# Kernel tuning notes

Measured on AMD Instinct MI355X. Metric: run time of the kernel, lower is better.

The kernel has to match this reference:

```python
import jax, jax.numpy as jnp
import numpy as np

N = 8192          # batch_size == number of graph nodes
F1 = 64
F2 = 64
D_IN = F1 * F2    # 4096, = int(sqrt(in_feats))**2
D_OUT = 4096      # out_feats, must equal F1*F2 for the final reshape
ALPHA = 0.2       # LeakyReLU negative slope


def setup_inputs() -> dict:
    key = jax.random.key(0)
    k_x, k_w, k_a = jax.random.split(key, 3)
    x = jax.random.normal(k_x, (N, F1, F2), dtype=jnp.float32)
    # torch Linear weight layout: [out_feats, in_feats]; xavier-uniform-ish scale
    lim_w = float(np.sqrt(6.0 / (D_IN + D_OUT)) * np.sqrt(2.0))
    W = jax.random.uniform(k_w, (D_OUT, D_IN), dtype=jnp.float32, minval=-lim_w, maxval=lim_w)
    lim_a = float(np.sqrt(6.0 / (1 + 2 * D_OUT)))
    a = jax.random.uniform(k_a, (1, 2 * D_OUT), dtype=jnp.float32, minval=-lim_a, maxval=lim_a)
    return {"x": x, "W": W, "a": a}


def reference(x, W, a):
    b, f1, f2 = x.shape
    x_flat = x.reshape(b, f1 * f2)                 # [N, D_in]
    h = x_flat @ W.T                               # [N, D_out]
    # scores[i,j] = leakyrelu(cat(h_i, h_j) @ a.T) = leakyrelu(h_i.a1 + h_j.a2)
    a1 = a[0, :D_OUT]                              # [D_out]
    a2 = a[0, D_OUT:]                              # [D_out]
    s1 = h @ a1                                    # [N]
    s2 = h @ a2                                    # [N]
    e = s1[:, None] + s2[None, :]                  # [N, N]
    e = jnp.where(e > 0, e, ALPHA * e)             # LeakyReLU
    attention = jax.nn.softmax(e, axis=-1)         # [N, N]
    # dropout=0.0 (eval-mode / deterministic reference)
    out = attention @ h                            # [N, D_out]
    return out.reshape(b, f1, f2)
```

## Files before the change

### kernel.cpp

```cpp
#include <hip/hip_runtime.h>
#include <hip/hip_bf16.h>
#include <stdint.h>


typedef float  f32x4  __attribute__((ext_vector_type(4)));
typedef __bf16 bf16x8 __attribute__((ext_vector_type(8)));

#define AS1 __attribute__((address_space(1)))
#define AS3 __attribute__((address_space(3)))

constexpr int NB  = 8192;
constexpr int DF  = 4096;
constexpr int CH  = 64;
constexpr int NCH = NB / CH;

constexpr int GK  = DF;
constexpr int BKK = 64;
constexpr int NT2 = GK / BKK;

__device__ __forceinline__ uint16_t f2bf_u(float f) {
  union { float f; uint32_t u; } x; x.f = f;
  return (uint16_t)((x.u + 0x7FFFu + ((x.u >> 16) & 1u)) >> 16);
}
__device__ __forceinline__ float bfu2f(uint16_t v) {
  union { uint32_t u; float f; } x; x.u = ((uint32_t)v) << 16;
  return x.f;
}

__global__ __launch_bounds__(256) void cvt_f32_to_bf16(
    const float* __restrict__ in, uint16_t* __restrict__ out, int n4,
    float* __restrict__ z1, float* __restrict__ z2, int zn) {
  int idx = blockIdx.x * 256 + threadIdx.x;
  int stride = gridDim.x * 256;
  if (z1) {
    for (int g = idx; g < zn; g += stride) { z1[g] = 0.f; z2[g] = 0.f; }
  }
  for (int i = idx; i < n4; i += stride) {
    float4 v = ((const float4*)in)[i];
    ushort4 o;
    o.x = f2bf_u(v.x); o.y = f2bf_u(v.y); o.z = f2bf_u(v.z); o.w = f2bf_u(v.w);
    ((ushort4*)out)[i] = o;
  }
}


#define STAGE_A(tt, half) do {                                                 \
  const uint16_t* g0_ = Ag + (size_t)((half) * 128) * GK + (size_t)(tt) * BKK; \
  uint32_t d_ = ((uint32_t)((tt) & 1)) * 32768u + (uint32_t)(half) * 8192u +   \
                (uint32_t)wave * 512u;                                         \
  __builtin_amdgcn_global_load_lds((const AS1 void*)g0_,                       \
      (AS3 void*)(lds + d_), 16, 0, 0);                                        \
  __builtin_amdgcn_global_load_lds((const AS1 void*)(g0_ + (size_t)64 * GK),   \
      (AS3 void*)(lds + d_ + 4096u), 16, 0, 0);                                \
} while (0)

#define STAGE_B(tt, half) do {                                                 \
  const uint16_t* g0_ = Bg + (size_t)((half) * 128) * GK + (size_t)(tt) * BKK; \
  uint32_t d_ = ((uint32_t)((tt) & 1)) * 32768u + 16384u +                     \
                (uint32_t)(half) * 8192u + (uint32_t)wave * 512u;              \
  __builtin_amdgcn_global_load_lds((const AS1 void*)g0_,                       \
      (AS3 void*)(lds + d_), 16, 0, 0);                                        \
  __builtin_amdgcn_global_load_lds((const AS1 void*)(g0_ + (size_t)64 * GK),   \
      (AS3 void*)(lds + d_ + 4096u), 16, 0, 0);                                \
} while (0)

#define LDA(mh) do {                                                           \
  _Pragma("unroll") for (int mf = 0; mf < 4; ++mf)                             \
    _Pragma("unroll") for (int ks = 0; ks < 2; ++ks)                           \
      aF[mf][ks] = *(const bf16x8*)(lds + bufo +                               \
          (uint32_t)(wm * 128 + (mh) * 64 + mf * 16 + lr) * 64u +              \
          (uint32_t)((ks * 32 + lg * 8) ^ swl));                               \
} while (0)

#define LDB(nh) do {                                                           \
  _Pragma("unroll") for (int nf = 0; nf < 2; ++nf)                             \
    _Pragma("unroll") for (int ks = 0; ks < 2; ++ks)                           \
      bF[nf][ks] = *(const bf16x8*)(lds + bufo + 16384u +                      \
          (uint32_t)(wn * 64 + (nh) * 32 + nf * 16 + lr) * 64u +               \
          (uint32_t)((ks * 32 + lg * 8) ^ swl));                               \
} while (0)

#define MMA(mh, nh) do {                                                       \
  _Pragma("unroll") for (int ks = 0; ks < 2; ++ks)                             \
    _Pragma("unroll") for (int mf = 0; mf < 4; ++mf)                           \
      _Pragma("unroll") for (int nf = 0; nf < 2; ++nf)                         \
        acc[(mh) * 4 + mf][(nh) * 2 + nf] =                                    \
            __builtin_amdgcn_mfma_f32_16x16x32_bf16(aF[mf][ks], bF[nf][ks],    \
                acc[(mh) * 4 + mf][(nh) * 2 + nf], 0, 0, 0);                   \
} while (0)

__global__ __launch_bounds__(512, 2) void gemm_nt_async(
    const uint16_t* __restrict__ A, const uint16_t* __restrict__ B,
    uint16_t* __restrict__ C, const float* __restrict__ a,
    float* __restrict__ s1g, float* __restrict__ s2g) {
  __shared__ uint16_t lds[65536];

  const int tid  = threadIdx.x;
  const int wave = tid >> 6;
  const int lane = tid & 63;
  const int lr   = lane & 15;
  const int lg   = lane >> 4;
  const int wm   = wave >> 2;
  const int wn   = wave & 3;
  const int swl  = (lr & 7) << 3;

  const int bid = blockIdx.x;
  const int swz = (bid & 7) * 64 + (bid >> 3);
  const int bx  = swz & 15;
  const int by  = swz >> 4;
  const int rowBase = by * 256;
  const int colBase = bx * 256;

  const int sr  = tid >> 3;
  const int sch = (tid & 7) ^ (sr & 7);
  const uint16_t* Ag = A + (size_t)(rowBase + sr) * GK + sch * 8;
  const uint16_t* Bg = B + (size_t)(colBase + sr) * GK + sch * 8;

  f32x4 acc[8][4];
#pragma unroll
  for (int mf = 0; mf < 8; ++mf)
#pragma unroll
    for (int nf = 0; nf < 4; ++nf) acc[mf][nf] = (f32x4){0.f, 0.f, 0.f, 0.f};

  STAGE_A(0, 0);
  STAGE_A(0, 1);
  STAGE_B(0, 0);
  STAGE_B(0, 1);
  asm volatile("s_waitcnt vmcnt(0)" ::: "memory");
  __builtin_amdgcn_s_barrier();

  bf16x8 aF[4][2], bF[2][2];

  for (int t = 0; t < NT2; ++t) {
    const uint32_t bufo = ((uint32_t)(t & 1)) * 32768u;

    if (t + 1 < NT2) {
      STAGE_A(t + 1, 0);
      STAGE_A(t + 1, 1);
      STAGE_B(t + 1, 0);
      STAGE_B(t + 1, 1);
    }

    LDA(0); LDB(0);
    MMA(0, 0);
    LDB(1);
    MMA(0, 1);
    LDA(1);
    MMA(1, 1);
    LDB(0);
    MMA(1, 0);

    if (t + 1 < NT2) {
      asm volatile("s_waitcnt vmcnt(0)" ::: "memory");
      __builtin_amdgcn_s_barrier();
    }
  }

  const int r0 = rowBase + wm * 128 + lg * 4;
  const int c0 = colBase + wn * 64 + lr;
#pragma unroll
  for (int mf = 0; mf < 8; ++mf)
#pragma unroll
    for (int nf = 0; nf < 4; ++nf)
#pragma unroll
      for (int e = 0; e < 4; ++e)
        C[(size_t)(r0 + mf * 16 + e) * (size_t)DF + (c0 + nf * 16)] =
            f2bf_u(acc[mf][nf][e]);

  float a1v[4], a2v[4];
#pragma unroll
  for (int nf = 0; nf < 4; ++nf) {
    int col = c0 + nf * 16;
    a1v[nf] = a[col];
    a2v[nf] = a[DF + col];
  }
#pragma unroll
  for (int mf = 0; mf < 8; ++mf) {
#pragma unroll
    for (int e = 0; e < 4; ++e) {
      float p1 = 0.f, p2 = 0.f;
#pragma unroll
      for (int nf = 0; nf < 4; ++nf) {
        float hv = acc[mf][nf][e];
        p1 += hv * a1v[nf];
        p2 += hv * a2v[nf];
      }
      p1 += __shfl_xor(p1, 1, 64); p1 += __shfl_xor(p1, 2, 64);
      p1 += __shfl_xor(p1, 4, 64); p1 += __shfl_xor(p1, 8, 64);
      p2 += __shfl_xor(p2, 1, 64); p2 += __shfl_xor(p2, 2, 64);
      p2 += __shfl_xor(p2, 4, 64); p2 += __shfl_xor(p2, 8, 64);
      if (lr == 0) {
        int row = r0 + mf * 16 + e;
        atomicAdd(&s1g[row], p1);
        atomicAdd(&s2g[row], p2);
      }
    }
  }
}

__global__ __launch_bounds__(256) void rankcount_kernel(
    const float* __restrict__ s1, const float* __restrict__ s2,
    int* __restrict__ pi, float* __restrict__ s2sorted, int* __restrict__ ci) {
  __shared__ float ld[NB];
  const int t = threadIdx.x;
  for (int idx = t; idx < NB; idx += 256) ld[idx] = s2[idx];
  __syncthreads();
  const int i    = blockIdx.x * 64 + (t >> 2);
  const int part = t & 3;
  const float v   = ld[i];
  const float thr = -s1[i];
  int cr = 0, cc = 0;
  const int q0 = part * (NB / 16);
  for (int q = q0; q < q0 + NB / 16; q++) {
    float4 u = ((const float4*)ld)[q];
    int jj = q * 4;
    cr += (u.x > v) || (u.x == v && (jj + 0) < i);
    cr += (u.y > v) || (u.y == v && (jj + 1) < i);
    cr += (u.z > v) || (u.z == v && (jj + 2) < i);
    cr += (u.w > v) || (u.w == v && (jj + 3) < i);
    cc += (u.x > thr) + (u.y > thr) + (u.z > thr) + (u.w > thr);
  }
  cr += __shfl_xor(cr, 1, 64); cr += __shfl_xor(cr, 2, 64);
  cc += __shfl_xor(cc, 1, 64); cc += __shfl_xor(cc, 2, 64);
  if (part == 0) {
    pi[cr] = i;
    s2sorted[cr] = v;
    ci[i] = cc;
  }
}

__global__ __launch_bounds__(256) void mega_kernel(
    const float* __restrict__ s2sorted, float* __restrict__ Sb,
    float* __restrict__ Sc, float* __restrict__ wbg, float* __restrict__ wcg,
    const float* __restrict__ s1, const int* __restrict__ ci,
    float* __restrict__ f1, float* __restrict__ f2,
    int* __restrict__ istart, int* __restrict__ cursor) {
  __shared__ float pb[256], pc[256];
  __shared__ int   histL[NB + 1];
  __shared__ int   ps[256];
  const int t = threadIdx.x;
  for (int g = t; g <= NB; g += 256) histL[g] = 0;

  float sb = 0.f, sc = 0.f;
  for (int c = t * 32; c < t * 32 + 32; c++) {
    float s = s2sorted[c];
    float wb = __expf(0.2f * s), wc = __expf(s);
    wbg[c] = wb; wcg[c] = wc;
    sb += wb; sc += wc;
  }
  pb[t] = sb; pc[t] = sc;
  __syncthreads();
  if (t == 0) {
    float rb = 0.f, rc = 0.f;
    for (int q = 0; q < 256; q++) {
      float tb = pb[q], tc = pc[q];
      pb[q] = rb; pc[q] = rc;
      rb += tb; rc += tc;
    }
    Sb[0] = 0.f; Sc[0] = 0.f;
    Sb[NB] = rb; Sc[NB] = rc;
  }
  __syncthreads();
  {
    float rb = pb[t], rc = pc[t];
    for (int c = t * 32; c < t * 32 + 32; c++) {
      rb += wbg[c]; rc += wcg[c];
      if (c + 1 < NB) { Sb[c + 1] = rb; Sc[c + 1] = rc; }
    }
  }
  __syncthreads();

  const float SbT = Sb[NB];
  for (int q = 0; q < NB / 256; q++) {
    int i = q * 256 + t;
    float s1i = s1[i];
    int c = ci[i];
    float q1 = __expf(0.2f * s1i), q2 = __expf(s1i);
    float l = q1 * (SbT - Sb[c]) + q2 * Sc[c];
    f1[i] = q1 / l;
    f2[i] = q2 / l;
    atomicAdd(&histL[c], 1);
  }
  __syncthreads();

  {
    const int lo = t * 33;
    const int hi = min(lo + 33, NB + 1);
    int s = 0;
    for (int b = lo; b < hi; b++) s += histL[b];
    ps[t] = s;
    __syncthreads();
    if (t == 0) {
      int r = 0;
      for (int q = 0; q < 256; q++) { int v = ps[q]; ps[q] = r; r += v; }
    }
    __syncthreads();
    int r = ps[t];
    for (int b = lo; b < hi; b++) { istart[b] = r; cursor[b] = r; r += histL[b]; }
    if (t == 255) istart[NB + 1] = r;
  }
}

__global__ __launch_bounds__(256) void pass1_kernel(
    const uint16_t* __restrict__ h, const int* __restrict__ pi,
    const float* __restrict__ wbg, const float* __restrict__ wcg,
    float* __restrict__ Bct, float* __restrict__ Cct,
    const int* __restrict__ ci, int* __restrict__ cursor,
    int* __restrict__ ilist) {
  __shared__ int   pj[CH];
  __shared__ float wb[CH], wc[CH];
  const int t  = threadIdx.x;
  const int cb = blockIdx.x;
  const int k  = blockIdx.y;
  const int flat = k * 4 + cb;
  if (flat < 32) {
    const int i = flat * 256 + t;
    const int b = ci[i];
    const int pos = atomicAdd(&cursor[b], 1);
    ilist[pos] = i;
  }
  if (t < CH) {
    int g = k * CH + t;
    pj[t] = pi[g]; wb[t] = wbg[g]; wc[t] = wcg[g];
  }
  __syncthreads();
  const int n0 = cb * 1024 + t * 4;
  float b0 = 0.f, b1 = 0.f, b2 = 0.f, b3 = 0.f;
  float c0 = 0.f, c1 = 0.f, c2 = 0.f, c3 = 0.f;
#pragma unroll 8
  for (int c = 0; c < CH; c++) {
    uint2 hv = *(const uint2*)(h + (size_t)pj[c] * DF + n0);
    float h0 = bfu2f((uint16_t)hv.x), h1 = bfu2f((uint16_t)(hv.x >> 16));
    float h2 = bfu2f((uint16_t)hv.y), h3 = bfu2f((uint16_t)(hv.y >> 16));
    float vb = wb[c], vc = wc[c];
    b0 += vb * h0; b1 += vb * h1; b2 += vb * h2; b3 += vb * h3;
    c0 += vc * h0; c1 += vc * h1; c2 += vc * h2; c3 += vc * h3;
  }
  *(float4*)(Bct + (size_t)k * DF + n0) = make_float4(b0, b1, b2, b3);
  *(float4*)(Cct + (size_t)k * DF + n0) = make_float4(c0, c1, c2, c3);
}

__global__ __launch_bounds__(256) void boff_kernel(
    const float* __restrict__ Bct, const float* __restrict__ Cct,
    float* __restrict__ Boff, float* __restrict__ Coff) {
  __shared__ float sB[4][64], sC[4][64];
  const int t   = threadIdx.x;
  const int cl  = t & 63;
  const int seg = t >> 6;
  const int col = blockIdx.x * 64 + cl;
  float sb = 0.f, sc = 0.f;
#pragma unroll 8
  for (int u = 0; u < NCH / 4; u++) {
    int kk = seg * (NCH / 4) + u;
    sb += Bct[(size_t)kk * DF + col];
    sc += Cct[(size_t)kk * DF + col];
  }
  sB[seg][cl] = sb; sC[seg][cl] = sc;
  __syncthreads();
  float rb = 0.f, rc = 0.f;
#pragma unroll
  for (int s = 0; s < 3; s++)
    if (s < seg) { rb += sB[s][cl]; rc += sC[s][cl]; }
#pragma unroll 4
  for (int u = 0; u < NCH / 4; u++) {
    int kk = seg * (NCH / 4) + u;
    Boff[(size_t)kk * DF + col] = rb;
    Coff[(size_t)kk * DF + col] = rc;
    rb += Bct[(size_t)kk * DF + col];
    rc += Cct[(size_t)kk * DF + col];
  }
  if (seg == 3) {
    Boff[(size_t)NCH * DF + col] = rb;
    Coff[(size_t)NCH * DF + col] = rc;
  }
}

__global__ __launch_bounds__(256) void pass2_kernel(
    const uint16_t* __restrict__ h, const int* __restrict__ pi,
    const float* __restrict__ wbg, const float* __restrict__ wcg,
    const float* __restrict__ Boff, const float* __restrict__ Coff,
    const int* __restrict__ istart, const int* __restrict__ ilist,
    const float* __restrict__ f1, const float* __restrict__ f2,
    float* __restrict__ out) {
  __shared__ int   pj[CH];
  __shared__ float wb[CH], wc[CH];
  __shared__ int   se[CH + 2];
  const int t  = threadIdx.x;
  const int cb = blockIdx.x;
  const int k  = blockIdx.y;
  if (t < CH) {
    int g = k * CH + t;
    pj[t] = pi[g]; wb[t] = wbg[g]; wc[t] = wcg[g];
  }
  if (t < CH + 2) se[t] = istart[k * CH + t];
  __syncthreads();
  const int n0 = cb * 1024 + t * 4;
  const float4 An = *(const float4*)(Boff + (size_t)NCH * DF + n0);
  const float4 Bo = *(const float4*)(Boff + (size_t)k * DF + n0);
  const float4 Co = *(const float4*)(Coff + (size_t)k * DF + n0);
  float b0 = Bo.x, b1 = Bo.y, b2 = Bo.z, b3 = Bo.w;
  float c0 = Co.x, c1 = Co.y, c2 = Co.z, c3 = Co.w;

  if (k == 0) {
    for (int idx = se[0]; idx < se[1]; idx++) {
      const int i = ilist[idx];
      const float fa = f1[i];
      *(float4*)(out + (size_t)i * DF + n0) =
          make_float4(fa * An.x, fa * An.y, fa * An.z, fa * An.w);
    }
  }
  for (int c = 0; c < CH; c++) {
    uint2 hv = *(const uint2*)(h + (size_t)pj[c] * DF + n0);
    float h0 = bfu2f((uint16_t)hv.x), h1 = bfu2f((uint16_t)(hv.x >> 16));
    float h2 = bfu2f((uint16_t)hv.y), h3 = bfu2f((uint16_t)(hv.y >> 16));
    float vb = wb[c], vc = wc[c];
    b0 += vb * h0; b1 += vb * h1; b2 += vb * h2; b3 += vb * h3;
    c0 += vc * h0; c1 += vc * h1; c2 += vc * h2; c3 += vc * h3;
    const int e0 = se[c + 1], e1 = se[c + 2];
    for (int idx = e0; idx < e1; idx++) {
      const int i = ilist[idx];
      const float fa = f1[i], fb = f2[i];
      *(float4*)(out + (size_t)i * DF + n0) = make_float4(
          fa * (An.x - b0) + fb * c0, fa * (An.y - b1) + fb * c1,
          fa * (An.z - b2) + fb * c2, fa * (An.w - b3) + fb * c3);
    }
  }
}

extern "C" void kernel_launch(void* const* d_in, const int* in_sizes, int n_in,
                              void* d_out, int out_size, void* d_ws, size_t ws_size,
                              hipStream_t stream) {
  const float* x = (const float*)d_in[0];
  const float* W = (const float*)d_in[1];
  const float* a = (const float*)d_in[2];
  float* out = (float*)d_out;

  char* ws = (char*)d_ws;
  uint16_t* h = (uint16_t*)ws;
  char* sm = ws + 67108864;
  float* s1       = (float*)(sm);
  float* s2       = (float*)(sm + 65536);
  float* s2sorted = (float*)(sm + 131072);
  int*   pi       = (int*)  (sm + 196608);
  int*   ci       = (int*)  (sm + 262144);
  float* Sb       = (float*)(sm + 327680);
  float* Sc       = (float*)(sm + 393216);
  float* wbg      = (float*)(sm + 458752);
  float* wcg      = (float*)(sm + 524288);
  float* f1       = (float*)(sm + 589824);
  float* f2       = (float*)(sm + 655360);
  int*   istart   = (int*)  (sm + 786432);
  int*   cursor   = (int*)  (sm + 851968);
  int*   ilist    = (int*)  (sm + 917504);
  float* Bct      = (float*)(sm + 1048576);
  float* Cct      = (float*)(sm + 3145728);
  float* Boff     = (float*)(sm + 5242880);
  float* Coff     = (float*)(sm + 7602176);
  char* base2 = ws + 67108864 + 10485760;
  uint16_t* xb = (uint16_t*)base2;
  uint16_t* Wb = (uint16_t*)(base2 + 67108864);

  cvt_f32_to_bf16<<<1024, 256, 0, stream>>>(x, xb, (NB * DF) / 4, s1, s2, NB);
  cvt_f32_to_bf16<<<1024, 256, 0, stream>>>(W, Wb, (DF * DF) / 4,
                                            nullptr, nullptr, 0);

  gemm_nt_async<<<(NB / 256) * (DF / 256), 512, 0, stream>>>(
      xb, Wb, h, a, s1, s2);

  rankcount_kernel<<<NB / 64, 256, 0, stream>>>(s1, s2, pi, s2sorted, ci);

  mega_kernel<<<1, 256, 0, stream>>>(s2sorted, Sb, Sc, wbg, wcg,
                                     s1, ci, f1, f2, istart, cursor);

  pass1_kernel<<<dim3(DF / 1024, NCH), 256, 0, stream>>>(
      h, pi, wbg, wcg, Bct, Cct, ci, cursor, ilist);

  boff_kernel<<<DF / 64, 256, 0, stream>>>(Bct, Cct, Boff, Coff);

  pass2_kernel<<<dim3(DF / 1024, NCH), 256, 0, stream>>>(
      h, pi, wbg, wcg, Boff, Coff, istart, ilist, f1, f2, out);
}
```

Measured before the change: 723.8 us.

## Fuse post-GEMM stages into one cooperative kernel with grid syncs

```diff
diff --git a/kernel.cpp b/kernel.cpp
--- a/kernel.cpp
+++ b/kernel.cpp
@@ -1,6 +1,9 @@
 #include <hip/hip_runtime.h>
 #include <hip/hip_bf16.h>
+#include <hip/hip_cooperative_groups.h>
 #include <stdint.h>
+
+namespace cg = cooperative_groups;
 
 
 typedef float  f32x4  __attribute__((ext_vector_type(4)));
@@ -27,19 +30,23 @@
   return x.f;
 }
 
-__global__ __launch_bounds__(256) void cvt_f32_to_bf16(
-    const float* __restrict__ in, uint16_t* __restrict__ out, int n4,
-    float* __restrict__ z1, float* __restrict__ z2, int zn) {
-  int idx = blockIdx.x * 256 + threadIdx.x;
-  int stride = gridDim.x * 256;
-  if (z1) {
-    for (int g = idx; g < zn; g += stride) { z1[g] = 0.f; z2[g] = 0.f; }
-  }
-  for (int i = idx; i < n4; i += stride) {
-    float4 v = ((const float4*)in)[i];
+__global__ __launch_bounds__(256) void cvt_all(
+    const float* __restrict__ x, uint16_t* __restrict__ xb,
+    const float* __restrict__ W, uint16_t* __restrict__ Wb) {
+  const int idx = blockIdx.x * 256 + threadIdx.x;
+  const int stride = gridDim.x * 256;
+  const int n4x = (NB * DF) / 4, n4w = (DF * DF) / 4;
+  for (int i = idx; i < n4x; i += stride) {
+    float4 v = ((const float4*)x)[i];
     ushort4 o;
     o.x = f2bf_u(v.x); o.y = f2bf_u(v.y); o.z = f2bf_u(v.z); o.w = f2bf_u(v.w);
-    ((ushort4*)out)[i] = o;
+    ((ushort4*)xb)[i] = o;
+  }
+  for (int i = idx; i < n4w; i += stride) {
+    float4 v = ((const float4*)W)[i];
+    ushort4 o;
+    o.x = f2bf_u(v.x); o.y = f2bf_u(v.y); o.z = f2bf_u(v.z); o.w = f2bf_u(v.w);
+    ((ushort4*)Wb)[i] = o;
   }
 }
 
@@ -92,7 +99,7 @@
 __global__ __launch_bounds__(512, 2) void gemm_nt_async(
     const uint16_t* __restrict__ A, const uint16_t* __restrict__ B,
     uint16_t* __restrict__ C, const float* __restrict__ a,
-    float* __restrict__ s1g, float* __restrict__ s2g) {
+    float* __restrict__ s1p, float* __restrict__ s2p) {
   __shared__ uint16_t lds[65536];
 
   const int tid  = threadIdx.x;
@@ -174,6 +181,7 @@
     a1v[nf] = a[col];
     a2v[nf] = a[DF + col];
   }
+  const int q = bx * 4 + wn;
 #pragma unroll
   for (int mf = 0; mf < 8; ++mf) {
 #pragma unroll
@@ -191,238 +199,247 @@
       p2 += __shfl_xor(p2, 4, 64); p2 += __shfl_xor(p2, 8, 64);
       if (lr == 0) {
         int row = r0 + mf * 16 + e;
-        atomicAdd(&s1g[row], p1);
-        atomicAdd(&s2g[row], p2);
-      }
-    }
-  }
-}
-
-__global__ __launch_bounds__(256) void rankcount_kernel(
-    const float* __restrict__ s1, const float* __restrict__ s2,
-    int* __restrict__ pi, float* __restrict__ s2sorted, int* __restrict__ ci) {
-  __shared__ float ld[NB];
-  const int t = threadIdx.x;
-  for (int idx = t; idx < NB; idx += 256) ld[idx] = s2[idx];
-  __syncthreads();
-  const int i    = blockIdx.x * 64 + (t >> 2);
-  const int part = t & 3;
-  const float v   = ld[i];
-  const float thr = -s1[i];
-  int cr = 0, cc = 0;
-  const int q0 = part * (NB / 16);
-  for (int q = q0; q < q0 + NB / 16; q++) {
-    float4 u = ((const float4*)ld)[q];
-    int jj = q * 4;
-    cr += (u.x > v) || (u.x == v && (jj + 0) < i);
-    cr += (u.y > v) || (u.y == v && (jj + 1) < i);
-    cr += (u.z > v) || (u.z == v && (jj + 2) < i);
-    cr += (u.w > v) || (u.w == v && (jj + 3) < i);
-    cc += (u.x > thr) + (u.y > thr) + (u.z > thr) + (u.w > thr);
-  }
-  cr += __shfl_xor(cr, 1, 64); cr += __shfl_xor(cr, 2, 64);
-  cc += __shfl_xor(cc, 1, 64); cc += __shfl_xor(cc, 2, 64);
-  if (part == 0) {
-    pi[cr] = i;
-    s2sorted[cr] = v;
-    ci[i] = cc;
-  }
-}
-
-__global__ __launch_bounds__(256) void mega_kernel(
-    const float* __restrict__ s2sorted, float* __restrict__ Sb,
-    float* __restrict__ Sc, float* __restrict__ wbg, float* __restrict__ wcg,
-    const float* __restrict__ s1, const int* __restrict__ ci,
-    float* __restrict__ f1, float* __restrict__ f2,
-    int* __restrict__ istart, int* __restrict__ cursor) {
-  __shared__ float pb[256], pc[256];
-  __shared__ int   histL[NB + 1];
-  __shared__ int   ps[256];
-  const int t = threadIdx.x;
-  for (int g = t; g <= NB; g += 256) histL[g] = 0;
-
-  float sb = 0.f, sc = 0.f;
-  for (int c = t * 32; c < t * 32 + 32; c++) {
-    float s = s2sorted[c];
-    float wb = __expf(0.2f * s), wc = __expf(s);
-    wbg[c] = wb; wcg[c] = wc;
-    sb += wb; sc += wc;
-  }
-  pb[t] = sb; pc[t] = sc;
-  __syncthreads();
-  if (t == 0) {
+        s1p[(size_t)q * NB + row] = p1;
+        s2p[(size_t)q * NB + row] = p2;
+      }
+    }
+  }
+}
+
+
+struct PostArgs {
+  const uint16_t* h;
+  const float* s1p; const float* s2p;
+  float* s1; float* s2;
+  int* pi; float* s2sorted; int* ci;
+  float* Sb; float* Sc; float* wbg; float* wcg;
+  float* f1; float* f2;
+  int* istart; int* cursor; int* ilist;
+  float* Bct; float* Cct; float* Boff; float* Coff;
+  float* out;
+};
+
+union PostSmem {
+  float ld[NB];
+  struct { float pb[256]; float pc[256]; int histL[NB + 1]; int ps[256]; } mg;
+  struct { int pj[CH]; float wb[CH]; float wc[CH]; int se[CH + 2]; } pp;
+  struct { float sB[4][64]; float sC[4][64]; } bo;
+};
+
+__global__ __launch_bounds__(256, 2) void gat_post(PostArgs P) {
+  __shared__ PostSmem smu;
+  cg::grid_group grid = cg::this_grid();
+  const int bid = blockIdx.x;
+  const int t   = threadIdx.x;
+
+  if (bid < 32) {
+    const int i = bid * 256 + t;
+    float v1 = 0.f, v2 = 0.f;
+#pragma unroll 16
+    for (int q = 0; q < 64; q++) {
+      v1 += P.s1p[(size_t)q * NB + i];
+      v2 += P.s2p[(size_t)q * NB + i];
+    }
+    P.s1[i] = v1;
+    P.s2[i] = v2;
+  }
+  grid.sync();
+
+  {
+    for (int idx = t; idx < NB; idx += 256) smu.ld[idx] = P.s2[idx];
+    __syncthreads();
+    const int i    = bid * 16 + (t >> 4);
+    const int part = t & 15;
+    const float v   = smu.ld[i];
+    const float thr = -P.s1[i];
+    int cr = 0, cc = 0;
+    const int q0 = part * (NB / 64);
+    for (int q = q0; q < q0 + NB / 64; q++) {
+      float4 u = ((const float4*)smu.ld)[q];
+      int jj = q * 4;
+      cr += (u.x > v) || (u.x == v && (jj + 0) < i);
+      cr += (u.y > v) || (u.y == v && (jj + 1) < i);
+      cr += (u.z > v) || (u.z == v && (jj + 2) < i);
+      cr += (u.w > v) || (u.w == v && (jj + 3) < i);
+      cc += (u.x > thr) + (u.y > thr) + (u.z > thr) + (u.w > thr);
+    }
+    cr += __shfl_xor(cr, 1, 64); cr += __shfl_xor(cr, 2, 64);
+    cr += __shfl_xor(cr, 4, 64); cr += __shfl_xor(cr, 8, 64);
+    cc += __shfl_xor(cc, 1, 64); cc += __shfl_xor(cc, 2, 64);
+    cc += __shfl_xor(cc, 4, 64); cc += __shfl_xor(cc, 8, 64);
+    if (part == 0) {
+      P.pi[cr] = i;
+      P.s2sorted[cr] = v;
+      P.ci[i] = cc;
+    }
+  }
+  grid.sync();
+
+  if (bid == 0) {
+    for (int g = t; g <= NB; g += 256) smu.mg.histL[g] = 0;
+    float sb = 0.f, sc = 0.f;
+    for (int c = t * 32; c < t * 32 + 32; c++) {
+      float s = P.s2sorted[c];
+      float wb = __expf(0.2f * s), wc = __expf(s);
+      P.wbg[c] = wb; P.wcg[c] = wc;
+      sb += wb; sc += wc;
+    }
+    smu.mg.pb[t] = sb; smu.mg.pc[t] = sc;
+    __syncthreads();
+    if (t == 0) {
+      float rb = 0.f, rc = 0.f;
+      for (int q = 0; q < 256; q++) {
+        float tb = smu.mg.pb[q], tc = smu.mg.pc[q];
+        smu.mg.pb[q] = rb; smu.mg.pc[q] = rc;
+        rb += tb; rc += tc;
+      }
+      P.Sb[0] = 0.f; P.Sc[0] = 0.f;
+      P.Sb[NB] = rb; P.Sc[NB] = rc;
+    }
+    __syncthreads();
+    {
+      float rb = smu.mg.pb[t], rc = smu.mg.pc[t];
+      for (int c = t * 32; c < t * 32 + 32; c++) {
+        rb += P.wbg[c]; rc += P.wcg[c];
+        if (c + 1 < NB) { P.Sb[c + 1] = rb; P.Sc[c + 1] = rc; }
+      }
+    }
+    __syncthreads();
+    const float SbT = P.Sb[NB];
+    for (int qq = 0; qq < NB / 256; qq++) {
+      int i = qq * 256 + t;
+      float s1i = P.s1[i];
+      int c = P.ci[i];
+      float q1 = __expf(0.2f * s1i), q2 = __expf(s1i);
+      float l = q1 * (SbT - P.Sb[c]) + q2 * P.Sc[c];
+      P.f1[i] = q1 / l;
+      P.f2[i] = q2 / l;
+      atomicAdd(&smu.mg.histL[c], 1);
+    }
+    __syncthreads();
+    {
+      const int lo = t * 33;
+      const int hi = min(lo + 33, NB + 1);
+      int s = 0;
+      for (int b = lo; b < hi; b++) s += smu.mg.histL[b];
+      smu.mg.ps[t] = s;
+      __syncthreads();
+      if (t == 0) {
+        int r = 0;
+        for (int q = 0; q < 256; q++) { int v = smu.mg.ps[q]; smu.mg.ps[q] = r; r += v; }
+      }
+      __syncthreads();
+      int r = smu.mg.ps[t];
+      for (int b = lo; b < hi; b++) {
+        P.istart[b] = r; P.cursor[b] = r; r += smu.mg.histL[b];
+      }
+      if (t == 255) P.istart[NB + 1] = r;
+    }
+  }
+  grid.sync();
+
+  {
+    const int cb = bid & 3;
+    const int k  = bid >> 2;
+    if (bid < 32) {
+      const int i = bid * 256 + t;
+      const int b = P.ci[i];
+      const int pos = atomicAdd(&P.cursor[b], 1);
+      P.ilist[pos] = i;
+    }
+    if (t < CH) {
+      int g = k * CH + t;
+      smu.pp.pj[t] = P.pi[g]; smu.pp.wb[t] = P.wbg[g]; smu.pp.wc[t] = P.wcg[g];
+    }
+    __syncthreads();
+    const int n0 = cb * 1024 + t * 4;
+    float b0 = 0.f, b1 = 0.f, b2 = 0.f, b3 = 0.f;
+    float c0 = 0.f, c1 = 0.f, c2 = 0.f, c3 = 0.f;
+#pragma unroll 8
+    for (int c = 0; c < CH; c++) {
+      uint2 hv = *(const uint2*)(P.h + (size_t)smu.pp.pj[c] * DF + n0);
+      float h0 = bfu2f((uint16_t)hv.x), h1 = bfu2f((uint16_t)(hv.x >> 16));
+      float h2 = bfu2f((uint16_t)hv.y), h3 = bfu2f((uint16_t)(hv.y >> 16));
+      float vb = smu.pp.wb[c], vc = smu.pp.wc[c];
+      b0 += vb * h0; b1 += vb * h1; b2 += vb * h2; b3 += vb * h3;
+      c0 += vc * h0; c1 += vc * h1; c2 += vc * h2; c3 += vc * h3;
+    }
+    *(float4*)(P.Bct + (size_t)k * DF + n0) = make_float4(b0, b1, b2, b3);
+    *(float4*)(P.Cct + (size_t)k * DF + n0) = make_float4(c0, c1, c2, c3);
+  }
+  grid.sync();
+
+  if (bid < 64) {
+    const int cl  = t & 63;
+    const int seg = t >> 6;
+    const int col = bid * 64 + cl;
+    float sb = 0.f, sc = 0.f;
+#pragma unroll 8
+    for (int u = 0; u < NCH / 4; u++) {
+      int kk = seg * (NCH / 4) + u;
+      sb += P.Bct[(size_t)kk * DF + col];
+      sc += P.Cct[(size_t)kk * DF + col];
+    }
+    smu.bo.sB[seg][cl] = sb; smu.bo.sC[seg][cl] = sc;
+    __syncthreads();
     float rb = 0.f, rc = 0.f;
-    for (int q = 0; q < 256; q++) {
-      float tb = pb[q], tc = pc[q];
-      pb[q] = rb; pc[q] = rc;
-      rb += tb; rc += tc;
-    }
-    Sb[0] = 0.f; Sc[0] = 0.f;
-    Sb[NB] = rb; Sc[NB] = rc;
-  }
-  __syncthreads();
+#pragma unroll
+    for (int s = 0; s < 3; s++)
+      if (s < seg) { rb += smu.bo.sB[s][cl]; rc += smu.bo.sC[s][cl]; }
+#pragma unroll 4
+    for (int u = 0; u < NCH / 4; u++) {
+      int kk = seg * (NCH / 4) + u;
+      P.Boff[(size_t)kk * DF + col] = rb;
+      P.Coff[(size_t)kk * DF + col] = rc;
+      rb += P.Bct[(size_t)kk * DF + col];
+      rc += P.Cct[(size_t)kk * DF + col];
+    }
+    if (seg == 3) {
+      P.Boff[(size_t)NCH * DF + col] = rb;
+      P.Coff[(size_t)NCH * DF + col] = rc;
+    }
+  }
+  grid.sync();
+
   {
-    float rb = pb[t], rc = pc[t];
-    for (int c = t * 32; c < t * 32 + 32; c++) {
-      rb += wbg[c]; rc += wcg[c];
-      if (c + 1 < NB) { Sb[c + 1] = rb; Sc[c + 1] = rc; }
-    }
-  }
-  __syncthreads();
-
-  const float SbT = Sb[NB];
-  for (int q = 0; q < NB / 256; q++) {
-    int i = q * 256 + t;
-    float s1i = s1[i];
-    int c = ci[i];
-    float q1 = __expf(0.2f * s1i), q2 = __expf(s1i);
-    float l = q1 * (SbT - Sb[c]) + q2 * Sc[c];
-    f1[i] = q1 / l;
-    f2[i] = q2 / l;
-    atomicAdd(&histL[c], 1);
-  }
-  __syncthreads();
-
-  {
-    const int lo = t * 33;
-    const int hi = min(lo + 33, NB + 1);
-    int s = 0;
-    for (int b = lo; b < hi; b++) s += histL[b];
-    ps[t] = s;
-    __syncthreads();
-    if (t == 0) {
-      int r = 0;
-      for (int q = 0; q < 256; q++) { int v = ps[q]; ps[q] = r; r += v; }
-    }
-    __syncthreads();
-    int r = ps[t];
-    for (int b = lo; b < hi; b++) { istart[b] = r; cursor[b] = r; r += histL[b]; }
-    if (t == 255) istart[NB + 1] = r;
-  }
-}
-
-__global__ __launch_bounds__(256) void pass1_kernel(
-    const uint16_t* __restrict__ h, const int* __restrict__ pi,
-    const float* __restrict__ wbg, const float* __restrict__ wcg,
-    float* __restrict__ Bct, float* __restrict__ Cct,
-    const int* __restrict__ ci, int* __restrict__ cursor,
-    int* __restrict__ ilist) {
-  __shared__ int   pj[CH];
-  __shared__ float wb[CH], wc[CH];
-  const int t  = threadIdx.x;
-  const int cb = blockIdx.x;
-  const int k  = blockIdx.y;
-  const int flat = k * 4 + cb;
-  if (flat < 32) {
-    const int i = flat * 256 + t;
-    const int b = ci[i];
-    const int pos = atomicAdd(&cursor[b], 1);
-    ilist[pos] = i;
-  }
-  if (t < CH) {
-    int g = k * CH + t;
-    pj[t] = pi[g]; wb[t] = wbg[g]; wc[t] = wcg[g];
-  }
-  __syncthreads();
-  const int n0 = cb * 1024 + t * 4;
-  float b0 = 0.f, b1 = 0.f, b2 = 0.f, b3 = 0.f;
-  float c0 = 0.f, c1 = 0.f, c2 = 0.f, c3 = 0.f;
-#pragma unroll 8
-  for (int c = 0; c < CH; c++) {
-    uint2 hv = *(const uint2*)(h + (size_t)pj[c] * DF + n0);
-    float h0 = bfu2f((uint16_t)hv.x), h1 = bfu2f((uint16_t)(hv.x >> 16));
-    float h2 = bfu2f((uint16_t)hv.y), h3 = bfu2f((uint16_t)(hv.y >> 16));
-    float vb = wb[c], vc = wc[c];
-    b0 += vb * h0; b1 += vb * h1; b2 += vb * h2; b3 += vb * h3;
-    c0 += vc * h0; c1 += vc * h1; c2 += vc * h2; c3 += vc * h3;
-  }
-  *(float4*)(Bct + (size_t)k * DF + n0) = make_float4(b0, b1, b2, b3);
-  *(float4*)(Cct + (size_t)k * DF + n0) = make_float4(c0, c1, c2, c3);
-}
-
-__global__ __launch_bounds__(256) void boff_kernel(
-    const float* __restrict__ Bct, const float* __restrict__ Cct,
-    float* __restrict__ Boff, float* __restrict__ Coff) {
-  __shared__ float sB[4][64], sC[4][64];
-  const int t   = threadIdx.x;
-  const int cl  = t & 63;
-  const int seg = t >> 6;
-  const int col = blockIdx.x * 64 + cl;
-  float sb = 0.f, sc = 0.f;
-#pragma unroll 8
-  for (int u = 0; u < NCH / 4; u++) {
-    int kk = seg * (NCH / 4) + u;
-    sb += Bct[(size_t)kk * DF + col];
-    sc += Cct[(size_t)kk * DF + col];
-  }
-  sB[seg][cl] = sb; sC[seg][cl] = sc;
-  __syncthreads();
-  float rb = 0.f, rc = 0.f;
-#pragma unroll
-  for (int s = 0; s < 3; s++)
-    if (s < seg) { rb += sB[s][cl]; rc += sC[s][cl]; }
-#pragma unroll 4
-  for (int u = 0; u < NCH / 4; u++) {
-    int kk = seg * (NCH / 4) + u;
-    Boff[(size_t)kk * DF + col] = rb;
-    Coff[(size_t)kk * DF + col] = rc;
-    rb += Bct[(size_t)kk * DF + col];
-    rc += Cct[(size_t)kk * DF + col];
-  }
-  if (seg == 3) {
-    Boff[(size_t)NCH * DF + col] = rb;
-    Coff[(size_t)NCH * DF + col] = rc;
-  }
-}
-
-__global__ __launch_bounds__(256) void pass2_kernel(
-    const uint16_t* __restrict__ h, const int* __restrict__ pi,
-    const float* __restrict__ wbg, const float* __restrict__ wcg,
-    const float* __restrict__ Boff, const float* __restrict__ Coff,
-    const int* __restrict__ istart, const int* __restrict__ ilist,
-    const float* __restrict__ f1, const float* __restrict__ f2,
-    float* __restrict__ out) {
-  __shared__ int   pj[CH];
-  __shared__ float wb[CH], wc[CH];
-  __shared__ int   se[CH + 2];
-  const int t  = threadIdx.x;
-  const int cb = blockIdx.x;
-  const int k  = blockIdx.y;
-  if (t < CH) {
-    int g = k * CH + t;
-    pj[t] = pi[g]; wb[t] = wbg[g]; wc[t] = wcg[g];
-  }
-  if (t < CH + 2) se[t] = istart[k * CH + t];
-  __syncthreads();
-  const int n0 = cb * 1024 + t * 4;
-  const float4 An = *(const float4*)(Boff + (size_t)NCH * DF + n0);
-  const float4 Bo = *(const float4*)(Boff + (size_t)k * DF + n0);
-  const float4 Co = *(const float4*)(Coff + (size_t)k * DF + n0);
-  float b0 = Bo.x, b1 = Bo.y, b2 = Bo.z, b3 = Bo.w;
-  float c0 = Co.x, c1 = Co.y, c2 = Co.z, c3 = Co.w;
-
-  if (k == 0) {
-    for (int idx = se[0]; idx < se[1]; idx++) {
-      const int i = ilist[idx];
-      const float fa = f1[i];
-      *(float4*)(out + (size_t)i * DF + n0) =
-          make_float4(fa * An.x, fa * An.y, fa * An.z, fa * An.w);
-    }
-  }
-  for (int c = 0; c < CH; c++) {
-    uint2 hv = *(const uint2*)(h + (size_t)pj[c] * DF + n0);
-    float h0 = bfu2f((uint16_t)hv.x), h1 = bfu2f((uint16_t)(hv.x >> 16));
-    float h2 = bfu2f((uint16_t)hv.y), h3 = bfu2f((uint16_t)(hv.y >> 16));
-    float vb = wb[c], vc = wc[c];
-    b0 += vb * h0; b1 += vb * h1; b2 += vb * h2; b3 += vb * h3;
-    c0 += vc * h0; c1 += vc * h1; c2 += vc * h2; c3 += vc * h3;
-    const int e0 = se[c + 1], e1 = se[c + 2];
-    for (int idx = e0; idx < e1; idx++) {
-      const int i = ilist[idx];
-      const float fa = f1[i], fb = f2[i];
-      *(float4*)(out + (size_t)i * DF + n0) = make_float4(
-          fa * (An.x - b0) + fb * c0, fa * (An.y - b1) + fb * c1,
-          fa * (An.z - b2) + fb * c2, fa * (An.w - b3) + fb * c3);
+    const int cb = bid & 3;
+    const int k  = bid >> 2;
+    if (t < CH) {
+      int g = k * CH + t;
+      smu.pp.pj[t] = P.pi[g]; smu.pp.wb[t] = P.wbg[g]; smu.pp.wc[t] = P.wcg[g];
+    }
+    if (t < CH + 2) smu.pp.se[t] = P.istart[k * CH + t];
+    __syncthreads();
+    const int n0 = cb * 1024 + t * 4;
+    const float4 An = *(const float4*)(P.Boff + (size_t)NCH * DF + n0);
+    const float4 Bo = *(const float4*)(P.Boff + (size_t)k * DF + n0);
+    const float4 Co = *(const float4*)(P.Coff + (size_t)k * DF + n0);
+    float b0 = Bo.x, b1 = Bo.y, b2 = Bo.z, b3 = Bo.w;
+    float c0 = Co.x, c1 = Co.y, c2 = Co.z, c3 = Co.w;
+
+    if (k == 0) {
+      for (int idx = smu.pp.se[0]; idx < smu.pp.se[1]; idx++) {
+        const int i = P.ilist[idx];
+        const float fa = P.f1[i];
+        *(float4*)(P.out + (size_t)i * DF + n0) =
+            make_float4(fa * An.x, fa * An.y, fa * An.z, fa * An.w);
+      }
+    }
+    for (int c = 0; c < CH; c++) {
+      uint2 hv = *(const uint2*)(P.h + (size_t)smu.pp.pj[c] * DF + n0);
+      float h0 = bfu2f((uint16_t)hv.x), h1 = bfu2f((uint16_t)(hv.x >> 16));
+      float h2 = bfu2f((uint16_t)hv.y), h3 = bfu2f((uint16_t)(hv.y >> 16));
+      float vb = smu.pp.wb[c], vc = smu.pp.wc[c];
+      b0 += vb * h0; b1 += vb * h1; b2 += vb * h2; b3 += vb * h3;
+      c0 += vc * h0; c1 += vc * h1; c2 += vc * h2; c3 += vc * h3;
+      const int e0 = smu.pp.se[c + 1], e1 = smu.pp.se[c + 2];
+      for (int idx = e0; idx < e1; idx++) {
+        const int i = P.ilist[idx];
+        const float fa = P.f1[i], fb = P.f2[i];
+        *(float4*)(P.out + (size_t)i * DF + n0) = make_float4(
+            fa * (An.x - b0) + fb * c0, fa * (An.y - b1) + fb * c1,
+            fa * (An.z - b2) + fb * c2, fa * (An.w - b3) + fb * c3);
+      }
     }
   }
 }
@@ -459,24 +476,23 @@
   char* base2 = ws + 67108864 + 10485760;
   uint16_t* xb = (uint16_t*)base2;
   uint16_t* Wb = (uint16_t*)(base2 + 67108864);
-
-  cvt_f32_to_bf16<<<1024, 256, 0, stream>>>(x, xb, (NB * DF) / 4, s1, s2, NB);
-  cvt_f32_to_bf16<<<1024, 256, 0, stream>>>(W, Wb, (DF * DF) / 4,
-                                            nullptr, nullptr, 0);
+  float* s1p = Bct;
+  float* s2p = Cct;
+
+  cvt_all<<<1024, 256, 0, stream>>>(x, xb, W, Wb);
 
   gemm_nt_async<<<(NB / 256) * (DF / 256), 512, 0, stream>>>(
-      xb, Wb, h, a, s1, s2);
-
-  rankcount_kernel<<<NB / 64, 256, 0, stream>>>(s1, s2, pi, s2sorted, ci);
-
-  mega_kernel<<<1, 256, 0, stream>>>(s2sorted, Sb, Sc, wbg, wcg,
-                                     s1, ci, f1, f2, istart, cursor);
-
-  pass1_kernel<<<dim3(DF / 1024, NCH), 256, 0, stream>>>(
-      h, pi, wbg, wcg, Bct, Cct, ci, cursor, ilist);
-
-  boff_kernel<<<DF / 64, 256, 0, stream>>>(Bct, Cct, Boff, Coff);
-
-  pass2_kernel<<<dim3(DF / 1024, NCH), 256, 0, stream>>>(
-      h, pi, wbg, wcg, Boff, Coff, istart, ilist, f1, f2, out);
-}
+      xb, Wb, h, a, s1p, s2p);
+
+  PostArgs P;
+  P.h = h; P.s1p = s1p; P.s2p = s2p; P.s1 = s1; P.s2 = s2;
+  P.pi = pi; P.s2sorted = s2sorted; P.ci = ci;
+  P.Sb = Sb; P.Sc = Sc; P.wbg = wbg; P.wcg = wcg;
+  P.f1 = f1; P.f2 = f2;
+  P.istart = istart; P.cursor = cursor; P.ilist = ilist;
+  P.Bct = Bct; P.Cct = Cct; P.Boff = Boff; P.Coff = Coff;
+  P.out = out;
+  void* kargs[] = { &P };
+  hipLaunchCooperativeKernel((const void*)gat_post, dim3(512), dim3(256),
+                             kargs, 0, stream);
+}
```

After: 1.012 ms. 1.4x slower.

## Fuse conversion kernels, replace score atomics with partial planes, overlap serial prefix with pass1

Applied to the files above, without the earlier changes.

```diff
diff --git a/kernel.cpp b/kernel.cpp
--- a/kernel.cpp
+++ b/kernel.cpp
@@ -27,19 +27,23 @@
   return x.f;
 }
 
-__global__ __launch_bounds__(256) void cvt_f32_to_bf16(
-    const float* __restrict__ in, uint16_t* __restrict__ out, int n4,
-    float* __restrict__ z1, float* __restrict__ z2, int zn) {
-  int idx = blockIdx.x * 256 + threadIdx.x;
-  int stride = gridDim.x * 256;
-  if (z1) {
-    for (int g = idx; g < zn; g += stride) { z1[g] = 0.f; z2[g] = 0.f; }
-  }
-  for (int i = idx; i < n4; i += stride) {
-    float4 v = ((const float4*)in)[i];
+__global__ __launch_bounds__(256) void cvt_all(
+    const float* __restrict__ x, uint16_t* __restrict__ xb,
+    const float* __restrict__ W, uint16_t* __restrict__ Wb) {
+  const int idx = blockIdx.x * 256 + threadIdx.x;
+  const int stride = gridDim.x * 256;
+  const int n4x = (NB * DF) / 4, n4w = (DF * DF) / 4;
+  for (int i = idx; i < n4x; i += stride) {
+    float4 v = ((const float4*)x)[i];
     ushort4 o;
     o.x = f2bf_u(v.x); o.y = f2bf_u(v.y); o.z = f2bf_u(v.z); o.w = f2bf_u(v.w);
-    ((ushort4*)out)[i] = o;
+    ((ushort4*)xb)[i] = o;
+  }
+  for (int i = idx; i < n4w; i += stride) {
+    float4 v = ((const float4*)W)[i];
+    ushort4 o;
+    o.x = f2bf_u(v.x); o.y = f2bf_u(v.y); o.z = f2bf_u(v.z); o.w = f2bf_u(v.w);
+    ((ushort4*)Wb)[i] = o;
   }
 }
 
@@ -92,7 +96,7 @@
 __global__ __launch_bounds__(512, 2) void gemm_nt_async(
     const uint16_t* __restrict__ A, const uint16_t* __restrict__ B,
     uint16_t* __restrict__ C, const float* __restrict__ a,
-    float* __restrict__ s1g, float* __restrict__ s2g) {
+    float* __restrict__ s1p, float* __restrict__ s2p) {
   __shared__ uint16_t lds[65536];
 
   const int tid  = threadIdx.x;
@@ -174,6 +178,7 @@
     a1v[nf] = a[col];
     a2v[nf] = a[DF + col];
   }
+  const int q = bx * 4 + wn;
 #pragma unroll
   for (int mf = 0; mf < 8; ++mf) {
 #pragma unroll
@@ -191,29 +196,49 @@
       p2 += __shfl_xor(p2, 4, 64); p2 += __shfl_xor(p2, 8, 64);
       if (lr == 0) {
         int row = r0 + mf * 16 + e;
-        atomicAdd(&s1g[row], p1);
-        atomicAdd(&s2g[row], p2);
+        s1p[(size_t)q * NB + row] = p1;
+        s2p[(size_t)q * NB + row] = p2;
       }
     }
   }
 }
 
 __global__ __launch_bounds__(256) void rankcount_kernel(
-    const float* __restrict__ s1, const float* __restrict__ s2,
-    int* __restrict__ pi, float* __restrict__ s2sorted, int* __restrict__ ci) {
+    const float* __restrict__ s1p, const float* __restrict__ s2p,
+    float* __restrict__ s1, int* __restrict__ pi,
+    float* __restrict__ s2sorted, int* __restrict__ ci,
+    float* __restrict__ wbg, float* __restrict__ wcg) {
   __shared__ float ld[NB];
-  const int t = threadIdx.x;
-  for (int idx = t; idx < NB; idx += 256) ld[idx] = s2[idx];
+  const int t   = threadIdx.x;
+  const int bid = blockIdx.x;
+
+  float accr[32];
+#pragma unroll
+  for (int j = 0; j < 32; j++) accr[j] = 0.f;
+  for (int q = 0; q < 64; q++) {
+    const float* plane = s2p + (size_t)q * NB;
+#pragma unroll
+    for (int j = 0; j < 32; j++) accr[j] += plane[t + 256 * j];
+  }
+#pragma unroll
+  for (int j = 0; j < 32; j++) ld[t + 256 * j] = accr[j];
+
+  const int i = bid * 64 + (t >> 2);
+  const int p = t & 3;
+  float s1v = 0.f;
+  for (int q = p * 16; q < p * 16 + 16; q++) s1v += s1p[(size_t)q * NB + i];
+  s1v += __shfl_xor(s1v, 1, 64);
+  s1v += __shfl_xor(s1v, 2, 64);
   __syncthreads();
-  const int i    = blockIdx.x * 64 + (t >> 2);
-  const int part = t & 3;
+
   const float v   = ld[i];
-  const float thr = -s1[i];
+  const float thr = -s1v;
   int cr = 0, cc = 0;
-  const int q0 = part * (NB / 16);
-  for (int q = q0; q < q0 + NB / 16; q++) {
-    float4 u = ((const float4*)ld)[q];
-    int jj = q * 4;
+  const int q0 = p * (NB / 16);
+  for (int it = 0; it < NB / 16; it++) {
+    int qq = q0 + ((it + p) & (NB / 16 - 1));
+    float4 u = ((const float4*)ld)[qq];
+    int jj = qq * 4;
     cr += (u.x > v) || (u.x == v && (jj + 0) < i);
     cr += (u.y > v) || (u.y == v && (jj + 1) < i);
     cr += (u.z > v) || (u.z == v && (jj + 2) < i);
@@ -222,106 +247,108 @@
   }
   cr += __shfl_xor(cr, 1, 64); cr += __shfl_xor(cr, 2, 64);
   cc += __shfl_xor(cc, 1, 64); cc += __shfl_xor(cc, 2, 64);
-  if (part == 0) {
+  if (p == 0) {
     pi[cr] = i;
     s2sorted[cr] = v;
     ci[i] = cc;
-  }
-}
-
-__global__ __launch_bounds__(256) void mega_kernel(
-    const float* __restrict__ s2sorted, float* __restrict__ Sb,
-    float* __restrict__ Sc, float* __restrict__ wbg, float* __restrict__ wcg,
+    s1[i] = s1v;
+    wbg[cr] = __expf(0.2f * v);
+    wcg[cr] = __expf(v);
+  }
+}
+
+union MpSmem {
+  struct { float pb[256]; float pc[256]; int histL[NB + 1]; int ps[256]; } mg;
+  struct { int pj[CH]; float wb[CH]; float wc[CH]; } pp;
+};
+
+__global__ __launch_bounds__(256) void megapass1_kernel(
+    const uint16_t* __restrict__ h, const int* __restrict__ pi,
+    const float* __restrict__ wbg, const float* __restrict__ wcg,
     const float* __restrict__ s1, const int* __restrict__ ci,
+    float* __restrict__ Sb, float* __restrict__ Sc,
     float* __restrict__ f1, float* __restrict__ f2,
-    int* __restrict__ istart, int* __restrict__ cursor) {
-  __shared__ float pb[256], pc[256];
-  __shared__ int   histL[NB + 1];
-  __shared__ int   ps[256];
-  const int t = threadIdx.x;
-  for (int g = t; g <= NB; g += 256) histL[g] = 0;
-
-  float sb = 0.f, sc = 0.f;
-  for (int c = t * 32; c < t * 32 + 32; c++) {
-    float s = s2sorted[c];
-    float wb = __expf(0.2f * s), wc = __expf(s);
-    wbg[c] = wb; wcg[c] = wc;
-    sb += wb; sc += wc;
-  }
-  pb[t] = sb; pc[t] = sc;
-  __syncthreads();
-  if (t == 0) {
-    float rb = 0.f, rc = 0.f;
-    for (int q = 0; q < 256; q++) {
-      float tb = pb[q], tc = pc[q];
-      pb[q] = rb; pc[q] = rc;
-      rb += tb; rc += tc;
-    }
-    Sb[0] = 0.f; Sc[0] = 0.f;
-    Sb[NB] = rb; Sc[NB] = rc;
-  }
-  __syncthreads();
-  {
-    float rb = pb[t], rc = pc[t];
-    for (int c = t * 32; c < t * 32 + 32; c++) {
-      rb += wbg[c]; rc += wcg[c];
-      if (c + 1 < NB) { Sb[c + 1] = rb; Sc[c + 1] = rc; }
-    }
-  }
-  __syncthreads();
-
-  const float SbT = Sb[NB];
-  for (int q = 0; q < NB / 256; q++) {
-    int i = q * 256 + t;
-    float s1i = s1[i];
-    int c = ci[i];
-    float q1 = __expf(0.2f * s1i), q2 = __expf(s1i);
-    float l = q1 * (SbT - Sb[c]) + q2 * Sc[c];
-    f1[i] = q1 / l;
-    f2[i] = q2 / l;
-    atomicAdd(&histL[c], 1);
-  }
-  __syncthreads();
-
-  {
-    const int lo = t * 33;
-    const int hi = min(lo + 33, NB + 1);
-    int s = 0;
-    for (int b = lo; b < hi; b++) s += histL[b];
-    ps[t] = s;
+    int* __restrict__ istart, int* __restrict__ ilist,
+    float* __restrict__ Bct, float* __restrict__ Cct) {
+  __shared__ MpSmem smu;
+  const int t   = threadIdx.x;
+  const int bid = blockIdx.x;
+
+  if (bid == 0) {
+    for (int g = t; g <= NB; g += 256) smu.mg.histL[g] = 0;
+    float sb = 0.f, sc = 0.f;
+    for (int c = t * 32; c < t * 32 + 32; c++) { sb += wbg[c]; sc += wcg[c]; }
+    smu.mg.pb[t] = sb; smu.mg.pc[t] = sc;
     __syncthreads();
     if (t == 0) {
-      int r = 0;
-      for (int q = 0; q < 256; q++) { int v = ps[q]; ps[q] = r; r += v; }
+      float rb = 0.f, rc = 0.f;
+      for (int q = 0; q < 256; q++) {
+        float tb = smu.mg.pb[q], tc = smu.mg.pc[q];
+        smu.mg.pb[q] = rb; smu.mg.pc[q] = rc;
+        rb += tb; rc += tc;
+      }
+      Sb[0] = 0.f; Sc[0] = 0.f;
+      Sb[NB] = rb; Sc[NB] = rc;
     }
     __syncthreads();
-    int r = ps[t];
-    for (int b = lo; b < hi; b++) { istart[b] = r; cursor[b] = r; r += histL[b]; }
-    if (t == 255) istart[NB + 1] = r;
-  }
-}
-
-__global__ __launch_bounds__(256) void pass1_kernel(
-    const uint16_t* __restrict__ h, const int* __restrict__ pi,
-    const float* __restrict__ wbg, const float* __restrict__ wcg,
-    float* __restrict__ Bct, float* __restrict__ Cct,
-    const int* __restrict__ ci, int* __restrict__ cursor,
-    int* __restrict__ ilist) {
-  __shared__ int   pj[CH];
-  __shared__ float wb[CH], wc[CH];
-  const int t  = threadIdx.x;
-  const int cb = blockIdx.x;
-  const int k  = blockIdx.y;
-  const int flat = k * 4 + cb;
-  if (flat < 32) {
-    const int i = flat * 256 + t;
-    const int b = ci[i];
-    const int pos = atomicAdd(&cursor[b], 1);
-    ilist[pos] = i;
-  }
+    {
+      float rb = smu.mg.pb[t], rc = smu.mg.pc[t];
+      for (int c = t * 32; c < t * 32 + 32; c++) {
+        rb += wbg[c]; rc += wcg[c];
+        if (c + 1 < NB) { Sb[c + 1] = rb; Sc[c + 1] = rc; }
+      }
+    }
+    __syncthreads();
+    const float SbT = Sb[NB];
+    for (int qq = 0; qq < NB / 256; qq++) {
+      int i = qq * 256 + t;
+      float s1i = s1[i];
+      int c = ci[i];
+      float q1 = __expf(0.2f * s1i), q2 = __expf(s1i);
+      float l = q1 * (SbT - Sb[c]) + q2 * Sc[c];
+      f1[i] = q1 / l;
+      f2[i] = q2 / l;
+      atomicAdd(&smu.mg.histL[c], 1);
+    }
+    __syncthreads();
+    {
+      const int lo = t * 33;
+      const int hi = min(lo + 33, NB + 1);
+      int s = 0;
+      for (int b = lo; b < hi; b++) s += smu.mg.histL[b];
+      smu.mg.ps[t] = s;
+      __syncthreads();
+      if (t == 0) {
+        int r = 0;
+        for (int q = 0; q < 256; q++) {
+          int v = smu.mg.ps[q]; smu.mg.ps[q] = r; r += v;
+        }
+      }
+      __syncthreads();
+      int r = smu.mg.ps[t];
+      for (int b = lo; b < hi; b++) {
+        istart[b] = r;
+        int hv = smu.mg.histL[b];
+        smu.mg.histL[b] = r;
+        r += hv;
+      }
+      if (t == 255) istart[NB + 1] = r;
+    }
+    __syncthreads();
+    for (int qq = 0; qq < NB / 256; qq++) {
+      int i = qq * 256 + t;
+      int pos = atomicAdd(&smu.mg.histL[ci[i]], 1);
+      ilist[pos] = i;
+    }
+    return;
+  }
+
+  const int fb = bid - 1;
+  const int cb = fb & 3;
+  const int k  = fb >> 2;
   if (t < CH) {
     int g = k * CH + t;
-    pj[t] = pi[g]; wb[t] = wbg[g]; wc[t] = wcg[g];
+    smu.pp.pj[t] = pi[g]; smu.pp.wb[t] = wbg[g]; smu.pp.wc[t] = wcg[g];
   }
   __syncthreads();
   const int n0 = cb * 1024 + t * 4;
@@ -329,10 +356,10 @@
   float c0 = 0.f, c1 = 0.f, c2 = 0.f, c3 = 0.f;
 #pragma unroll 8
   for (int c = 0; c < CH; c++) {
-    uint2 hv = *(const uint2*)(h + (size_t)pj[c] * DF + n0);
+    uint2 hv = *(const uint2*)(h + (size_t)smu.pp.pj[c] * DF + n0);
     float h0 = bfu2f((uint16_t)hv.x), h1 = bfu2f((uint16_t)(hv.x >> 16));
     float h2 = bfu2f((uint16_t)hv.y), h3 = bfu2f((uint16_t)(hv.y >> 16));
-    float vb = wb[c], vc = wc[c];
+    float vb = smu.pp.wb[c], vc = smu.pp.wc[c];
     b0 += vb * h0; b1 += vb * h1; b2 += vb * h2; b3 += vb * h3;
     c0 += vc * h0; c1 += vc * h1; c2 += vc * h2; c3 += vc * h3;
   }
@@ -439,7 +466,6 @@
   uint16_t* h = (uint16_t*)ws;
   char* sm = ws + 67108864;
   float* s1       = (float*)(sm);
-  float* s2       = (float*)(sm + 65536);
   float* s2sorted = (float*)(sm + 131072);
   int*   pi       = (int*)  (sm + 196608);
   int*   ci       = (int*)  (sm + 262144);
@@ -450,7 +476,6 @@
   float* f1       = (float*)(sm + 589824);
   float* f2       = (float*)(sm + 655360);
   int*   istart   = (int*)  (sm + 786432);
-  int*   cursor   = (int*)  (sm + 851968);
   int*   ilist    = (int*)  (sm + 917504);
   float* Bct      = (float*)(sm + 1048576);
   float* Cct      = (float*)(sm + 3145728);
@@ -459,21 +484,19 @@
   char* base2 = ws + 67108864 + 10485760;
   uint16_t* xb = (uint16_t*)base2;
   uint16_t* Wb = (uint16_t*)(base2 + 67108864);
-
-  cvt_f32_to_bf16<<<1024, 256, 0, stream>>>(x, xb, (NB * DF) / 4, s1, s2, NB);
-  cvt_f32_to_bf16<<<1024, 256, 0, stream>>>(W, Wb, (DF * DF) / 4,
-                                            nullptr, nullptr, 0);
+  float* s1p = Bct;
+  float* s2p = Cct;
+
+  cvt_all<<<1024, 256, 0, stream>>>(x, xb, W, Wb);
 
   gemm_nt_async<<<(NB / 256) * (DF / 256), 512, 0, stream>>>(
-      xb, Wb, h, a, s1, s2);
-
-  rankcount_kernel<<<NB / 64, 256, 0, stream>>>(s1, s2, pi, s2sorted, ci);
-
-  mega_kernel<<<1, 256, 0, stream>>>(s2sorted, Sb, Sc, wbg, wcg,
-                                     s1, ci, f1, f2, istart, cursor);
-
-  pass1_kernel<<<dim3(DF / 1024, NCH), 256, 0, stream>>>(
-      h, pi, wbg, wcg, Bct, Cct, ci, cursor, ilist);
+      xb, Wb, h, a, s1p, s2p);
+
+  rankcount_kernel<<<NB / 64, 256, 0, stream>>>(
+      s1p, s2p, s1, pi, s2sorted, ci, wbg, wcg);
+
+  megapass1_kernel<<<1 + (DF / 1024) * NCH, 256, 0, stream>>>(
+      h, pi, wbg, wcg, s1, ci, Sb, Sc, f1, f2, istart, ilist, Bct, Cct);
 
   boff_kernel<<<DF / 64, 256, 0, stream>>>(Bct, Cct, Boff, Coff);
 
```

Result: slower. 771.8 us (+6.6%).
